# Kernel optimization log

Measured on AMD Instinct MI355X. Metric: run time of the kernel, lower is better.

The kernel has to match this reference:

```python
import jax, jax.numpy as jnp
import numpy as np

N, M, D, DV = 8192, 8192, 128, 128
N_MASK = 1_000_000


def setup_inputs() -> dict:
    key = jax.random.key(0)
    kq, kk, kv, kr, kc = jax.random.split(key, 5)
    query = jax.random.normal(kq, (N, D), dtype=jnp.float32)
    k = jax.random.normal(kk, (M, D), dtype=jnp.float32)
    value = jax.random.normal(kv, (M, DV), dtype=jnp.float32)
    mask_rows = jax.random.randint(kr, (N_MASK,), 0, N, dtype=jnp.int64 if jax.config.jax_enable_x64 else jnp.int32)
    mask_cols = jax.random.randint(kc, (N_MASK,), 0, M, dtype=jnp.int64 if jax.config.jax_enable_x64 else jnp.int32)
    return {"query": query, "key": k, "value": value,
            "mask_rows": mask_rows, "mask_cols": mask_cols}


def reference(query, key, value, mask_rows, mask_cols):
    d = query.shape[1]
    # [N, M] score matrix: q @ k^T / sqrt(d)
    scores = (query @ key.T) / jnp.sqrt(jnp.asarray(d, dtype=query.dtype))
    # scatter -inf at masked coordinates (torch: scaled[mask[0], mask[1]] = -inf)
    scores = scores.at[mask_rows, mask_cols].set(-jnp.inf)
    attn = jax.nn.softmax(scores, axis=1)
    return attn @ value
```

## Files before the change

kernel.cpp:

```cpp
#include <hip/hip_runtime.h>
#include <stdint.h>

#define NQ 8192
#define NM 8192
#define DD 128
#define DVD 128
#define BK 64
#define NKB64 (NM / BK)
#define BQ 128
#define NQB (NQ / BQ)
#define NSPLIT 12

typedef float f32x4 __attribute__((ext_vector_type(4)));
typedef short s16x8 __attribute__((ext_vector_type(8)));
typedef __fp16 fp16x2 __attribute__((ext_vector_type(2)));
union FragU { uint32_t u[4]; s16x8 v; };
union H2U { fp16x2 h; uint32_t u; };

__device__ __forceinline__ uint32_t bf16rne(float x) {
  uint32_t u = __float_as_uint(x);
  return (u + 0x7FFFu + ((u >> 16) & 1u)) >> 16;
}
__device__ __forceinline__ uint32_t pk2(float a, float b) {
  return __builtin_amdgcn_perm(__float_as_uint(b) + 0x8000u,
                               __float_as_uint(a) + 0x8000u, 0x07060302u);
}

__device__ __forceinline__ void glds16(const void* g, void* l) {
  __builtin_amdgcn_global_load_lds((const __attribute__((address_space(1))) uint32_t*)g,
                                   (__attribute__((address_space(3))) uint32_t*)l, 16, 0, 0);
}

#define SZ_MASK ((size_t)(NM / 64) * NQ * 8)
#define OFF_K   (SZ_MASK)
#define SZ_KB   ((size_t)NM * DD * 2)
#define OFF_V   (OFF_K + SZ_KB)
#define OFF_OP  (OFF_V + SZ_KB)
#define SZ_OPH  ((size_t)NQ * DVD * 2)
#define OFF_L   (OFF_OP + (size_t)NSPLIT * SZ_OPH)

__global__ __launch_bounds__(256) void conv_scatter_kernel(
    const float* __restrict__ K, const float* __restrict__ V,
    uint8_t* __restrict__ Kswz, uint8_t* __restrict__ Vtswz,
    const int* __restrict__ mr, const int* __restrict__ mc, int nmask,
    unsigned int* __restrict__ maskT) {
  __shared__ float Vf[64][132];
  int b = blockIdx.x;
  int tid = threadIdx.x;
  if (b < 512) {
    int t = b * 256 + tid;
    int key = t >> 4, c = t & 15;
    const float* s = K + (size_t)key * DD + 8 * c;
    float4 a = *(const float4*)s, bb = *(const float4*)(s + 4);
    uint4 d;
    d.x = bf16rne(a.x) | (bf16rne(a.y) << 16);
    d.y = bf16rne(a.z) | (bf16rne(a.w) << 16);
    d.z = bf16rne(bb.x) | (bf16rne(bb.y) << 16);
    d.w = bf16rne(bb.z) | (bf16rne(bb.w) << 16);
    size_t off = (size_t)(key >> 6) * 16384 + (size_t)(key & 63) * 256 +
                 (size_t)((c ^ (key & 15)) << 4);
    *(uint4*)(Kswz + off) = d;
  } else if (b < 640) {
    int kb = b - 512;
#pragma unroll
    for (int i = 0; i < 8; ++i) {
      int idx = tid + 256 * i;
      int key = idx >> 5, c4 = idx & 31;
      float4 f = *(const float4*)(V + ((size_t)kb * 64 + key) * DVD + 4 * c4);
      *(float4*)&Vf[key][4 * c4] = f;
    }
    __syncthreads();
#pragma unroll
    for (int j = 0; j < 4; ++j) {
      int s = tid + 256 * j;
      int dv = s >> 3, c = s & 7;
      uint4 d;
      uint32_t* dw = (uint32_t*)&d;
#pragma unroll
      for (int w = 0; w < 4; ++w) {
        int k0 = 8 * c + 2 * w;
        dw[w] = bf16rne(Vf[k0][dv]) | (bf16rne(Vf[k0 + 1][dv]) << 16);
      }
      size_t off = (size_t)kb * 16384 + (size_t)dv * 128 + (size_t)((c ^ (dv & 7)) << 4);
      *(uint4*)(Vtswz + off) = d;
    }
  } else {
    size_t i = (size_t)(b - 640) * 256 + tid;
    if (i < (size_t)nmask) {
      int r = mr[i], c = mc[i];
      size_t w = ((size_t)(c >> 6) * NQ + r) * 2 + ((c >> 5) & 1);
      atomicOr(&maskT[w], 1u << (c & 31));
    }
  }
}

__global__ __launch_bounds__(256, 3) void attn_kernel(
    const float* __restrict__ Q, const uint8_t* __restrict__ Kswz,
    const uint8_t* __restrict__ Vtswz, const unsigned int* __restrict__ maskT,
    __fp16* __restrict__ Opart, float* __restrict__ lsum) {
  const int bid = blockIdx.x;
  const int span = bid % NSPLIT;
  const int qblk = bid / NSPLIT;
  const int niter = (span < 8) ? 11 : 10;
  const int kb0 = (span < 8) ? span * 11 : 88 + (span - 8) * 10;

  const int tid = threadIdx.x;
  const int wid = tid >> 6, lane = tid & 63;
  const int g = lane >> 4, qi = lane & 15;
  const int qw = qblk * BQ + wid * 32;

  __shared__ uint8_t Klds[16384];
  __shared__ uint8_t Vlds[16384];
  __shared__ uint32_t Psc[4][16][32];

  const float SC = 0.08838834764831845f * 1.4426950408889634f;

  s16x8 qfrag[2][4];
#pragma unroll
  for (int qt = 0; qt < 2; ++qt)
#pragma unroll
    for (int ks = 0; ks < 4; ++ks) {
      const float* qs = Q + (size_t)(qw + 16 * qt + qi) * DD + 32 * ks + 8 * g;
      float4 a = *(const float4*)qs, b = *(const float4*)(qs + 4);
      FragU fu;
      fu.u[0] = bf16rne(a.x * SC) | (bf16rne(a.y * SC) << 16);
      fu.u[1] = bf16rne(a.z * SC) | (bf16rne(a.w * SC) << 16);
      fu.u[2] = bf16rne(b.x * SC) | (bf16rne(b.y * SC) << 16);
      fu.u[3] = bf16rne(b.z * SC) | (bf16rne(b.w * SC) << 16);
      qfrag[qt][ks] = fu.v;
    }

  f32x4 accO[8][2];
#pragma unroll
  for (int dt = 0; dt < 8; ++dt)
#pragma unroll
    for (int qt = 0; qt < 2; ++qt) accO[dt][qt] = (f32x4)0.f;
  f32x4 accL[2] = {(f32x4)0.f, (f32x4)0.f};
  const f32x4 z4 = (f32x4)0.f;

  FragU onesu;
  onesu.u[0] = onesu.u[1] = onesu.u[2] = onesu.u[3] = 0x3F803F80u;
  const s16x8 onesfrag = onesu.v;

  const s16x8* Kv = (const s16x8*)Klds;
  const s16x8* Vv = (const s16x8*)Vlds;
  const s16x8* kp[4];
#pragma unroll
  for (int ks = 0; ks < 4; ++ks) kp[ks] = Kv + qi * 16 + ((g + 4 * ks) ^ qi);
  const s16x8* vp[2];
#pragma unroll
  for (int kh = 0; kh < 2; ++kh) vp[kh] = Vv + qi * 8 + ((4 * kh + g) ^ (qi & 7));
  uint32_t* pw = &Psc[wid][qi][0];
  uint32_t* wr[4];
#pragma unroll
  for (int kt = 0; kt < 4; ++kt) wr[kt] = &pw[2 * ((4 * kt + g) ^ qi)];
  const uint32_t* rd[4];
#pragma unroll
  for (int kh = 0; kh < 2; ++kh)
#pragma unroll
    for (int hb = 0; hb < 2; ++hb) rd[2 * kh + hb] = &pw[2 * ((8 * kh + 2 * g + hb) ^ qi)];

  const uint8_t* ktp = Kswz + (size_t)kb0 * 16384 + (size_t)tid * 16;
  const uint8_t* vtp = Vtswz + (size_t)kb0 * 16384 + (size_t)tid * 16;
  uint8_t* kld = Klds + wid * 1024;
  uint8_t* vld = Vlds + wid * 1024;
  const uint2* mp0 = (const uint2*)maskT + (size_t)kb0 * NQ + qw + qi;
  const uint2* mp1 = mp0 + 16;

  for (int it = 0; it < niter; ++it) {
    __syncthreads();
#pragma unroll
    for (int s = 0; s < 4; ++s) {
      glds16(ktp + s * 4096, kld + s * 4096);
      glds16(vtp + s * 4096, vld + s * 4096);
    }
    uint2 wm0 = *mp0, wm1 = *mp1;
    ktp += 16384; vtp += 16384; mp0 += NQ; mp1 += NQ;
    __syncthreads();

    f32x4 sf[2][4];
#pragma unroll
    for (int kt = 0; kt < 4; ++kt) {
      {
        s16x8 kf = kp[0][kt * 256];
        sf[0][kt] = __builtin_amdgcn_mfma_f32_16x16x32_bf16(kf, qfrag[0][0], z4, 0, 0, 0);
        sf[1][kt] = __builtin_amdgcn_mfma_f32_16x16x32_bf16(kf, qfrag[1][0], z4, 0, 0, 0);
      }
#pragma unroll
      for (int ks = 1; ks < 4; ++ks) {
        s16x8 kf = kp[ks][kt * 256];
        sf[0][kt] = __builtin_amdgcn_mfma_f32_16x16x32_bf16(kf, qfrag[0][ks], sf[0][kt], 0, 0, 0);
        sf[1][kt] = __builtin_amdgcn_mfma_f32_16x16x32_bf16(kf, qfrag[1][ks], sf[1][kt], 0, 0, 0);
      }
    }

    if (__ballot((wm0.x | wm0.y | wm1.x | wm1.y) != 0)) {
#pragma unroll
      for (int qt = 0; qt < 2; ++qt) {
        uint2 wm = qt ? wm1 : wm0;
#pragma unroll
        for (int kt = 0; kt < 4; ++kt)
#pragma unroll
          for (int r = 0; r < 4; ++r) {
            int kl = 16 * kt + 4 * g + r;
            unsigned int w = (kl & 32) ? wm.y : wm.x;
            if ((w >> (kl & 31)) & 1u) sf[qt][kt][r] = -3.0e38f;
          }
      }
    }

    s16x8 pfrag[2][2];
#pragma unroll
    for (int qt = 0; qt < 2; ++qt) {
#pragma unroll
      for (int kt = 0; kt < 4; ++kt) {
        float p0 = __builtin_amdgcn_exp2f(sf[qt][kt][0]);
        float p1 = __builtin_amdgcn_exp2f(sf[qt][kt][1]);
        float p2 = __builtin_amdgcn_exp2f(sf[qt][kt][2]);
        float p3 = __builtin_amdgcn_exp2f(sf[qt][kt][3]);
        uint2 pk;
        pk.x = pk2(p0, p1);
        pk.y = pk2(p2, p3);
        *(uint2*)wr[kt] = pk;
      }
      FragU pf0, pf1;
      uint2 a0 = *(const uint2*)rd[0];
      uint2 b0 = *(const uint2*)rd[1];
      uint2 a1 = *(const uint2*)rd[2];
      uint2 b1 = *(const uint2*)rd[3];
      pf0.u[0] = a0.x; pf0.u[1] = a0.y; pf0.u[2] = b0.x; pf0.u[3] = b0.y;
      pf1.u[0] = a1.x; pf1.u[1] = a1.y; pf1.u[2] = b1.x; pf1.u[3] = b1.y;
      pfrag[qt][0] = pf0.v;
      pfrag[qt][1] = pf1.v;
    }

#pragma unroll
    for (int kh = 0; kh < 2; ++kh) {
      accL[0] = __builtin_amdgcn_mfma_f32_16x16x32_bf16(onesfrag, pfrag[0][kh], accL[0], 0, 0, 0);
      accL[1] = __builtin_amdgcn_mfma_f32_16x16x32_bf16(onesfrag, pfrag[1][kh], accL[1], 0, 0, 0);
    }

#pragma unroll
    for (int dt = 0; dt < 8; ++dt) {
#pragma unroll
      for (int kh = 0; kh < 2; ++kh) {
        s16x8 vf = vp[kh][dt * 128];
        accO[dt][0] = __builtin_amdgcn_mfma_f32_16x16x32_bf16(vf, pfrag[0][kh], accO[dt][0], 0, 0, 0);
        accO[dt][1] = __builtin_amdgcn_mfma_f32_16x16x32_bf16(vf, pfrag[1][kh], accO[dt][1], 0, 0, 0);
      }
    }
  }

#pragma unroll
  for (int qt = 0; qt < 2; ++qt) {
    int q = qw + 16 * qt + qi;
#pragma unroll
    for (int dt = 0; dt < 8; ++dt) {
      H2U h0, h1;
      h0.h = __builtin_amdgcn_cvt_pkrtz(accO[dt][qt][0], accO[dt][qt][1]);
      h1.h = __builtin_amdgcn_cvt_pkrtz(accO[dt][qt][2], accO[dt][qt][3]);
      uint2 st = {h0.u, h1.u};
      *(uint2*)(Opart + ((size_t)span * NQ + q) * DVD + 16 * dt + 4 * g) = st;
    }
    if (g == 0) lsum[(size_t)span * NQ + q] = accL[qt][0];
  }
}

__global__ __launch_bounds__(256) void merge_kernel(const __fp16* __restrict__ Opart,
                                                    const float* __restrict__ lsum,
                                                    float* __restrict__ out) {
  int idx = blockIdx.x * 256 + threadIdx.x;
  int row = idx >> 5, c4 = idx & 31;
  float den = 0.f;
  f32x4 o = (f32x4)0.f;
#pragma unroll
  for (int p = 0; p < NSPLIT; ++p) {
    den += lsum[(size_t)p * NQ + row];
    uint2 h = *(const uint2*)(Opart + ((size_t)p * NQ + row) * DVD + 4 * c4);
    H2U a, b;
    a.u = h.x; b.u = h.y;
    o[0] += (float)a.h[0]; o[1] += (float)a.h[1];
    o[2] += (float)b.h[0]; o[3] += (float)b.h[1];
  }
  o *= (1.f / den);
  ((f32x4*)out)[idx] = o;
}

extern "C" void kernel_launch(void* const* d_in, const int* in_sizes, int n_in,
                              void* d_out, int out_size, void* d_ws, size_t ws_size,
                              hipStream_t stream) {
  const float* Q = (const float*)d_in[0];
  const float* K = (const float*)d_in[1];
  const float* V = (const float*)d_in[2];
  const int* mr = (const int*)d_in[3];
  const int* mc = (const int*)d_in[4];
  const int nmask = in_sizes[3];

  uint8_t* ws = (uint8_t*)d_ws;
  unsigned int* maskT = (unsigned int*)ws;
  uint8_t* Kswz = ws + OFF_K;
  uint8_t* Vtswz = ws + OFF_V;
  __fp16* Opart = (__fp16*)(ws + OFF_OP);
  float* lsum = (float*)(ws + OFF_L);

  hipMemsetAsync(maskT, 0, SZ_MASK, stream);
  conv_scatter_kernel<<<640 + (nmask + 255) / 256, 256, 0, stream>>>(
      K, V, Kswz, Vtswz, mr, mc, nmask, maskT);
  attn_kernel<<<NQB * NSPLIT, 256, 0, stream>>>(Q, Kswz, Vtswz, maskT, Opart, lsum);
  merge_kernel<<<NQ * DVD / 4 / 256, 256, 0, stream>>>(Opart, lsum, (float*)d_out);
}
```

Measured before the change: 170.2 us.

## Fuse memset, conversion, scatter, attention and merge into one cooperative kernel

Replaces the memset plus three kernel launches with a single cooperative persistent kernel. It uses grid-wide syncs between the phases: mask zeroing with K/V conversion, mask scatter, split attention, and merge. The aim is to remove launch gaps and per-kernel tail drain. The grid is sized from a runtime occupancy query, so the split count is 12 or 8, and the old multi-kernel path remains as a fallback. In exchange, every grid barrier makes all blocks wait on the slowest one. The occupancy query also runs on the host each call, and the merge loop now takes a runtime split count instead of a compile-time one.

```diff
diff --git a/kernel.cpp b/kernel.cpp
--- a/kernel.cpp
+++ b/kernel.cpp
@@ -1,15 +1,15 @@
 #include <hip/hip_runtime.h>
+#include <hip/hip_cooperative_groups.h>
 #include <stdint.h>
+
+namespace cg = cooperative_groups;
 
 #define NQ 8192
 #define NM 8192
 #define DD 128
 #define DVD 128
-#define BK 64
-#define NKB64 (NM / BK)
-#define BQ 128
-#define NQB (NQ / BQ)
-#define NSPLIT 12
+#define NQB 64
+#define NSPLX 12
 
 typedef float f32x4 __attribute__((ext_vector_type(4)));
 typedef short s16x8 __attribute__((ext_vector_type(8)));
@@ -25,7 +25,6 @@
   return __builtin_amdgcn_perm(__float_as_uint(b) + 0x8000u,
                                __float_as_uint(a) + 0x8000u, 0x07060302u);
 }
-
 __device__ __forceinline__ void glds16(const void* g, void* l) {
   __builtin_amdgcn_global_load_lds((const __attribute__((address_space(1))) uint32_t*)g,
                                    (__attribute__((address_space(3))) uint32_t*)l, 16, 0, 0);
@@ -37,18 +36,183 @@
 #define OFF_V   (OFF_K + SZ_KB)
 #define OFF_OP  (OFF_V + SZ_KB)
 #define SZ_OPH  ((size_t)NQ * DVD * 2)
-#define OFF_L   (OFF_OP + (size_t)NSPLIT * SZ_OPH)
-
-__global__ __launch_bounds__(256) void conv_scatter_kernel(
-    const float* __restrict__ K, const float* __restrict__ V,
-    uint8_t* __restrict__ Kswz, uint8_t* __restrict__ Vtswz,
-    const int* __restrict__ mr, const int* __restrict__ mc, int nmask,
-    unsigned int* __restrict__ maskT) {
-  __shared__ float Vf[64][132];
-  int b = blockIdx.x;
-  int tid = threadIdx.x;
-  if (b < 512) {
-    int t = b * 256 + tid;
+#define OFF_L   (OFF_OP + (size_t)NSPLX * SZ_OPH)
+
+struct AttnPtrs {
+  const float* Q;
+  const uint8_t* Kswz;
+  const uint8_t* Vtswz;
+  const unsigned int* maskT;
+  __fp16* Opart;
+  float* lsum;
+};
+
+__device__ __forceinline__ void attn_body(const AttnPtrs& P, uint8_t* smem,
+                                          int tid, int qblk, int span, int kb0,
+                                          int niter) {
+  const int wid = tid >> 6, lane = tid & 63;
+  const int g = lane >> 4, qi = lane & 15;
+  const int qw = qblk * 128 + wid * 32;
+
+  const float SC = 0.08838834764831845f * 1.4426950408889634f;
+
+  s16x8 qfrag[2][4];
+#pragma unroll
+  for (int qt = 0; qt < 2; ++qt)
+#pragma unroll
+    for (int ks = 0; ks < 4; ++ks) {
+      const float* qs = P.Q + (size_t)(qw + 16 * qt + qi) * DD + 32 * ks + 8 * g;
+      float4 a = *(const float4*)qs, b = *(const float4*)(qs + 4);
+      FragU fu;
+      fu.u[0] = bf16rne(a.x * SC) | (bf16rne(a.y * SC) << 16);
+      fu.u[1] = bf16rne(a.z * SC) | (bf16rne(a.w * SC) << 16);
+      fu.u[2] = bf16rne(b.x * SC) | (bf16rne(b.y * SC) << 16);
+      fu.u[3] = bf16rne(b.z * SC) | (bf16rne(b.w * SC) << 16);
+      qfrag[qt][ks] = fu.v;
+    }
+
+  f32x4 accO[8][2];
+#pragma unroll
+  for (int dt = 0; dt < 8; ++dt)
+#pragma unroll
+    for (int qt = 0; qt < 2; ++qt) accO[dt][qt] = (f32x4)0.f;
+  f32x4 accL[2] = {(f32x4)0.f, (f32x4)0.f};
+  const f32x4 z4 = (f32x4)0.f;
+
+  FragU onesu;
+  onesu.u[0] = onesu.u[1] = onesu.u[2] = onesu.u[3] = 0x3F803F80u;
+  const s16x8 onesfrag = onesu.v;
+
+  const s16x8* Kv = (const s16x8*)smem;
+  const s16x8* Vv = (const s16x8*)(smem + 16384);
+  const s16x8* kp[4];
+#pragma unroll
+  for (int ks = 0; ks < 4; ++ks) kp[ks] = Kv + qi * 16 + ((g + 4 * ks) ^ qi);
+  const s16x8* vp[2];
+#pragma unroll
+  for (int kh = 0; kh < 2; ++kh) vp[kh] = Vv + qi * 8 + ((4 * kh + g) ^ (qi & 7));
+  uint32_t* pw = (uint32_t*)(smem + 32768) + (wid * 16 + qi) * 32;
+  uint32_t* wr[4];
+#pragma unroll
+  for (int kt = 0; kt < 4; ++kt) wr[kt] = &pw[2 * ((4 * kt + g) ^ qi)];
+  const uint32_t* rd[4];
+#pragma unroll
+  for (int kh = 0; kh < 2; ++kh)
+#pragma unroll
+    for (int hb = 0; hb < 2; ++hb) rd[2 * kh + hb] = &pw[2 * ((8 * kh + 2 * g + hb) ^ qi)];
+
+  const uint8_t* ktp = P.Kswz + (size_t)kb0 * 16384 + (size_t)tid * 16;
+  const uint8_t* vtp = P.Vtswz + (size_t)kb0 * 16384 + (size_t)tid * 16;
+  uint8_t* kld = smem + wid * 1024;
+  uint8_t* vld = smem + 16384 + wid * 1024;
+  const uint2* mp0 = (const uint2*)P.maskT + (size_t)kb0 * NQ + qw + qi;
+  const uint2* mp1 = mp0 + 16;
+
+  for (int it = 0; it < niter; ++it) {
+    __syncthreads();
+#pragma unroll
+    for (int s = 0; s < 4; ++s) {
+      glds16(ktp + s * 4096, kld + s * 4096);
+      glds16(vtp + s * 4096, vld + s * 4096);
+    }
+    uint2 wm0 = *mp0, wm1 = *mp1;
+    ktp += 16384; vtp += 16384; mp0 += NQ; mp1 += NQ;
+    __syncthreads();
+
+    f32x4 sf[2][4];
+#pragma unroll
+    for (int kt = 0; kt < 4; ++kt) {
+      {
+        s16x8 kf = kp[0][kt * 256];
+        sf[0][kt] = __builtin_amdgcn_mfma_f32_16x16x32_bf16(kf, qfrag[0][0], z4, 0, 0, 0);
+        sf[1][kt] = __builtin_amdgcn_mfma_f32_16x16x32_bf16(kf, qfrag[1][0], z4, 0, 0, 0);
+      }
+#pragma unroll
+      for (int ks = 1; ks < 4; ++ks) {
+        s16x8 kf = kp[ks][kt * 256];
+        sf[0][kt] = __builtin_amdgcn_mfma_f32_16x16x32_bf16(kf, qfrag[0][ks], sf[0][kt], 0, 0, 0);
+        sf[1][kt] = __builtin_amdgcn_mfma_f32_16x16x32_bf16(kf, qfrag[1][ks], sf[1][kt], 0, 0, 0);
+      }
+    }
+
+    if (__ballot((wm0.x | wm0.y | wm1.x | wm1.y) != 0)) {
+#pragma unroll
+      for (int qt = 0; qt < 2; ++qt) {
+        uint2 wm = qt ? wm1 : wm0;
+#pragma unroll
+        for (int kt = 0; kt < 4; ++kt)
+#pragma unroll
+          for (int r = 0; r < 4; ++r) {
+            int kl = 16 * kt + 4 * g + r;
+            unsigned int w = (kl & 32) ? wm.y : wm.x;
+            if ((w >> (kl & 31)) & 1u) sf[qt][kt][r] = -3.0e38f;
+          }
+      }
+    }
+
+    s16x8 pfrag[2][2];
+#pragma unroll
+    for (int qt = 0; qt < 2; ++qt) {
+#pragma unroll
+      for (int kt = 0; kt < 4; ++kt) {
+        float p0 = __builtin_amdgcn_exp2f(sf[qt][kt][0]);
+        float p1 = __builtin_amdgcn_exp2f(sf[qt][kt][1]);
+        float p2 = __builtin_amdgcn_exp2f(sf[qt][kt][2]);
+        float p3 = __builtin_amdgcn_exp2f(sf[qt][kt][3]);
+        uint2 pk;
+        pk.x = pk2(p0, p1);
+        pk.y = pk2(p2, p3);
+        *(uint2*)wr[kt] = pk;
+      }
+      FragU pf0, pf1;
+      uint2 a0 = *(const uint2*)rd[0];
+      uint2 b0 = *(const uint2*)rd[1];
+      uint2 a1 = *(const uint2*)rd[2];
+      uint2 b1 = *(const uint2*)rd[3];
+      pf0.u[0] = a0.x; pf0.u[1] = a0.y; pf0.u[2] = b0.x; pf0.u[3] = b0.y;
+      pf1.u[0] = a1.x; pf1.u[1] = a1.y; pf1.u[2] = b1.x; pf1.u[3] = b1.y;
+      pfrag[qt][0] = pf0.v;
+      pfrag[qt][1] = pf1.v;
+    }
+
+#pragma unroll
+    for (int kh = 0; kh < 2; ++kh) {
+      accL[0] = __builtin_amdgcn_mfma_f32_16x16x32_bf16(onesfrag, pfrag[0][kh], accL[0], 0, 0, 0);
+      accL[1] = __builtin_amdgcn_mfma_f32_16x16x32_bf16(onesfrag, pfrag[1][kh], accL[1], 0, 0, 0);
+    }
+
+#pragma unroll
+    for (int dt = 0; dt < 8; ++dt) {
+#pragma unroll
+      for (int kh = 0; kh < 2; ++kh) {
+        s16x8 vf = vp[kh][dt * 128];
+        accO[dt][0] = __builtin_amdgcn_mfma_f32_16x16x32_bf16(vf, pfrag[0][kh], accO[dt][0], 0, 0, 0);
+        accO[dt][1] = __builtin_amdgcn_mfma_f32_16x16x32_bf16(vf, pfrag[1][kh], accO[dt][1], 0, 0, 0);
+      }
+    }
+  }
+
+#pragma unroll
+  for (int qt = 0; qt < 2; ++qt) {
+    int q = qw + 16 * qt + qi;
+#pragma unroll
+    for (int dt = 0; dt < 8; ++dt) {
+      H2U h0, h1;
+      h0.h = __builtin_amdgcn_cvt_pkrtz(accO[dt][qt][0], accO[dt][qt][1]);
+      h1.h = __builtin_amdgcn_cvt_pkrtz(accO[dt][qt][2], accO[dt][qt][3]);
+      uint2 st = {h0.u, h1.u};
+      *(uint2*)(P.Opart + ((size_t)span * NQ + q) * DVD + 16 * dt + 4 * g) = st;
+    }
+    if (g == 0) P.lsum[(size_t)span * NQ + q] = accL[qt][0];
+  }
+}
+
+__device__ __forceinline__ void conv_vblock(int vb, int tid, const float* K,
+                                            const float* V, uint8_t* Kswz,
+                                            uint8_t* Vtswz, unsigned int* maskT,
+                                            uint8_t* smem) {
+  if (vb < 512) {
+    int t = vb * 256 + tid;
     int key = t >> 4, c = t & 15;
     const float* s = K + (size_t)key * DD + 8 * c;
     float4 a = *(const float4*)s, bb = *(const float4*)(s + 4);
@@ -60,8 +224,9 @@
     size_t off = (size_t)(key >> 6) * 16384 + (size_t)(key & 63) * 256 +
                  (size_t)((c ^ (key & 15)) << 4);
     *(uint4*)(Kswz + off) = d;
-  } else if (b < 640) {
-    int kb = b - 512;
+  } else if (vb < 640) {
+    float(*Vf)[132] = (float(*)[132])smem;
+    int kb = vb - 512;
 #pragma unroll
     for (int i = 0; i < 8; ++i) {
       int idx = tid + 256 * i;
@@ -84,6 +249,82 @@
       size_t off = (size_t)kb * 16384 + (size_t)dv * 128 + (size_t)((c ^ (dv & 7)) << 4);
       *(uint4*)(Vtswz + off) = d;
     }
+    __syncthreads();
+  } else {
+    uint4* m4 = (uint4*)maskT;
+    int i0 = (vb - 640) * 256 + tid;
+    uint4 z = {0, 0, 0, 0};
+#pragma unroll
+    for (int j = 0; j < 16; ++j) m4[i0 + j * 32768] = z;
+  }
+}
+
+__global__ __launch_bounds__(256, 3) void fused_kernel(
+    const float* __restrict__ Q, const float* __restrict__ K,
+    const float* __restrict__ V, const int* __restrict__ mr,
+    const int* __restrict__ mc, int nmask, uint8_t* __restrict__ Kswz,
+    uint8_t* __restrict__ Vtswz, unsigned int* __restrict__ maskT,
+    __fp16* __restrict__ Opart, float* __restrict__ lsum,
+    float* __restrict__ out, int nsplit) {
+  cg::grid_group grid = cg::this_grid();
+  const int bid = blockIdx.x;
+  const int tid = threadIdx.x;
+  const int nthr = gridDim.x * 256;
+  __shared__ uint8_t smem[40960];
+
+  for (int vb = bid; vb < 768; vb += gridDim.x)
+    conv_vblock(vb, tid, K, V, Kswz, Vtswz, maskT, smem);
+  __threadfence();
+  grid.sync();
+
+  for (int i = bid * 256 + tid; i < nmask; i += nthr) {
+    int r = mr[i], c = mc[i];
+    size_t w = ((size_t)(c >> 6) * NQ + r) * 2 + ((c >> 5) & 1);
+    atomicOr(&maskT[w], 1u << (c & 31));
+  }
+  __threadfence();
+  grid.sync();
+
+  {
+    const int span = bid % nsplit;
+    const int qblk = bid / nsplit;
+    const int base = 128 / nsplit;
+    const int rem = 128 - base * nsplit;
+    const int niter = base + (span < rem ? 1 : 0);
+    const int kb0 = span * base + (span < rem ? span : rem);
+    AttnPtrs P = {Q, Kswz, Vtswz, maskT, Opart, lsum};
+    attn_body(P, smem, tid, qblk, span, kb0, niter);
+  }
+  __threadfence();
+  grid.sync();
+
+  for (int idx = bid * 256 + tid; idx < NQ * DVD / 4; idx += nthr) {
+    int row = idx >> 5, c4 = idx & 31;
+    float den = 0.f;
+    f32x4 o = (f32x4)0.f;
+    for (int p = 0; p < nsplit; ++p) {
+      den += lsum[(size_t)p * NQ + row];
+      uint2 h = *(const uint2*)(Opart + ((size_t)p * NQ + row) * DVD + 4 * c4);
+      H2U a, b;
+      a.u = h.x; b.u = h.y;
+      o[0] += (float)a.h[0]; o[1] += (float)a.h[1];
+      o[2] += (float)b.h[0]; o[3] += (float)b.h[1];
+    }
+    o *= (1.f / den);
+    ((f32x4*)out)[idx] = o;
+  }
+}
+
+__global__ __launch_bounds__(256) void conv_scatter_kernel(
+    const float* __restrict__ K, const float* __restrict__ V,
+    uint8_t* __restrict__ Kswz, uint8_t* __restrict__ Vtswz,
+    const int* __restrict__ mr, const int* __restrict__ mc, int nmask,
+    unsigned int* __restrict__ maskT) {
+  __shared__ uint8_t smem[40960];
+  int b = blockIdx.x;
+  int tid = threadIdx.x;
+  if (b < 640) {
+    conv_vblock(b, tid, K, V, Kswz, Vtswz, maskT, smem);
   } else {
     size_t i = (size_t)(b - 640) * 256 + tid;
     if (i < (size_t)nmask) {
@@ -98,172 +339,14 @@
     const float* __restrict__ Q, const uint8_t* __restrict__ Kswz,
     const uint8_t* __restrict__ Vtswz, const unsigned int* __restrict__ maskT,
     __fp16* __restrict__ Opart, float* __restrict__ lsum) {
+  __shared__ uint8_t smem[40960];
   const int bid = blockIdx.x;
-  const int span = bid % NSPLIT;
-  const int qblk = bid / NSPLIT;
+  const int span = bid % 12;
+  const int qblk = bid / 12;
   const int niter = (span < 8) ? 11 : 10;
   const int kb0 = (span < 8) ? span * 11 : 88 + (span - 8) * 10;
-
-  const int tid = threadIdx.x;
-  const int wid = tid >> 6, lane = tid & 63;
-  const int g = lane >> 4, qi = lane & 15;
-  const int qw = qblk * BQ + wid * 32;
-
-  __shared__ uint8_t Klds[16384];
-  __shared__ uint8_t Vlds[16384];
-  __shared__ uint32_t Psc[4][16][32];
-
-  const float SC = 0.08838834764831845f * 1.4426950408889634f;
-
-  s16x8 qfrag[2][4];
-#pragma unroll
-  for (int qt = 0; qt < 2; ++qt)
-#pragma unroll
-    for (int ks = 0; ks < 4; ++ks) {
-      const float* qs = Q + (size_t)(qw + 16 * qt + qi) * DD + 32 * ks + 8 * g;
-      float4 a = *(const float4*)qs, b = *(const float4*)(qs + 4);
-      FragU fu;
-      fu.u[0] = bf16rne(a.x * SC) | (bf16rne(a.y * SC) << 16);
-      fu.u[1] = bf16rne(a.z * SC) | (bf16rne(a.w * SC) << 16);
-      fu.u[2] = bf16rne(b.x * SC) | (bf16rne(b.y * SC) << 16);
-      fu.u[3] = bf16rne(b.z * SC) | (bf16rne(b.w * SC) << 16);
-      qfrag[qt][ks] = fu.v;
-    }
-
-  f32x4 accO[8][2];
-#pragma unroll
-  for (int dt = 0; dt < 8; ++dt)
-#pragma unroll
-    for (int qt = 0; qt < 2; ++qt) accO[dt][qt] = (f32x4)0.f;
-  f32x4 accL[2] = {(f32x4)0.f, (f32x4)0.f};
-  const f32x4 z4 = (f32x4)0.f;
-
-  FragU onesu;
-  onesu.u[0] = onesu.u[1] = onesu.u[2] = onesu.u[3] = 0x3F803F80u;
-  const s16x8 onesfrag = onesu.v;
-
-  const s16x8* Kv = (const s16x8*)Klds;
-  const s16x8* Vv = (const s16x8*)Vlds;
-  const s16x8* kp[4];
-#pragma unroll
-  for (int ks = 0; ks < 4; ++ks) kp[ks] = Kv + qi * 16 + ((g + 4 * ks) ^ qi);
-  const s16x8* vp[2];
-#pragma unroll
-  for (int kh = 0; kh < 2; ++kh) vp[kh] = Vv + qi * 8 + ((4 * kh + g) ^ (qi & 7));
-  uint32_t* pw = &Psc[wid][qi][0];
-  uint32_t* wr[4];
-#pragma unroll
-  for (int kt = 0; kt < 4; ++kt) wr[kt] = &pw[2 * ((4 * kt + g) ^ qi)];
-  const uint32_t* rd[4];
-#pragma unroll
-  for (int kh = 0; kh < 2; ++kh)
-#pragma unroll
-    for (int hb = 0; hb < 2; ++hb) rd[2 * kh + hb] = &pw[2 * ((8 * kh + 2 * g + hb) ^ qi)];
-
-  const uint8_t* ktp = Kswz + (size_t)kb0 * 16384 + (size_t)tid * 16;
-  const uint8_t* vtp = Vtswz + (size_t)kb0 * 16384 + (size_t)tid * 16;
-  uint8_t* kld = Klds + wid * 1024;
-  uint8_t* vld = Vlds + wid * 1024;
-  const uint2* mp0 = (const uint2*)maskT + (size_t)kb0 * NQ + qw + qi;
-  const uint2* mp1 = mp0 + 16;
-
-  for (int it = 0; it < niter; ++it) {
-    __syncthreads();
-#pragma unroll
-    for (int s = 0; s < 4; ++s) {
-      glds16(ktp + s * 4096, kld + s * 4096);
-      glds16(vtp + s * 4096, vld + s * 4096);
-    }
-    uint2 wm0 = *mp0, wm1 = *mp1;
-    ktp += 16384; vtp += 16384; mp0 += NQ; mp1 += NQ;
-    __syncthreads();
-
-    f32x4 sf[2][4];
-#pragma unroll
-    for (int kt = 0; kt < 4; ++kt) {
-      {
-        s16x8 kf = kp[0][kt * 256];
-        sf[0][kt] = __builtin_amdgcn_mfma_f32_16x16x32_bf16(kf, qfrag[0][0], z4, 0, 0, 0);
-        sf[1][kt] = __builtin_amdgcn_mfma_f32_16x16x32_bf16(kf, qfrag[1][0], z4, 0, 0, 0);
-      }
-#pragma unroll
-      for (int ks = 1; ks < 4; ++ks) {
-        s16x8 kf = kp[ks][kt * 256];
-        sf[0][kt] = __builtin_amdgcn_mfma_f32_16x16x32_bf16(kf, qfrag[0][ks], sf[0][kt], 0, 0, 0);
-        sf[1][kt] = __builtin_amdgcn_mfma_f32_16x16x32_bf16(kf, qfrag[1][ks], sf[1][kt], 0, 0, 0);
-      }
-    }
-
-    if (__ballot((wm0.x | wm0.y | wm1.x | wm1.y) != 0)) {
-#pragma unroll
-      for (int qt = 0; qt < 2; ++qt) {
-        uint2 wm = qt ? wm1 : wm0;
-#pragma unroll
-        for (int kt = 0; kt < 4; ++kt)
-#pragma unroll
-          for (int r = 0; r < 4; ++r) {
-            int kl = 16 * kt + 4 * g + r;
-            unsigned int w = (kl & 32) ? wm.y : wm.x;
-            if ((w >> (kl & 31)) & 1u) sf[qt][kt][r] = -3.0e38f;
-          }
-      }
-    }
-
-    s16x8 pfrag[2][2];
-#pragma unroll
-    for (int qt = 0; qt < 2; ++qt) {
-#pragma unroll
-      for (int kt = 0; kt < 4; ++kt) {
-        float p0 = __builtin_amdgcn_exp2f(sf[qt][kt][0]);
-        float p1 = __builtin_amdgcn_exp2f(sf[qt][kt][1]);
-        float p2 = __builtin_amdgcn_exp2f(sf[qt][kt][2]);
-        float p3 = __builtin_amdgcn_exp2f(sf[qt][kt][3]);
-        uint2 pk;
-        pk.x = pk2(p0, p1);
-        pk.y = pk2(p2, p3);
-        *(uint2*)wr[kt] = pk;
-      }
-      FragU pf0, pf1;
-      uint2 a0 = *(const uint2*)rd[0];
-      uint2 b0 = *(const uint2*)rd[1];
-      uint2 a1 = *(const uint2*)rd[2];
-      uint2 b1 = *(const uint2*)rd[3];
-      pf0.u[0] = a0.x; pf0.u[1] = a0.y; pf0.u[2] = b0.x; pf0.u[3] = b0.y;
-      pf1.u[0] = a1.x; pf1.u[1] = a1.y; pf1.u[2] = b1.x; pf1.u[3] = b1.y;
-      pfrag[qt][0] = pf0.v;
-      pfrag[qt][1] = pf1.v;
-    }
-
-#pragma unroll
-    for (int kh = 0; kh < 2; ++kh) {
-      accL[0] = __builtin_amdgcn_mfma_f32_16x16x32_bf16(onesfrag, pfrag[0][kh], accL[0], 0, 0, 0);
-      accL[1] = __builtin_amdgcn_mfma_f32_16x16x32_bf16(onesfrag, pfrag[1][kh], accL[1], 0, 0, 0);
-    }
-
-#pragma unroll
-    for (int dt = 0; dt < 8; ++dt) {
-#pragma unroll
-      for (int kh = 0; kh < 2; ++kh) {
-        s16x8 vf = vp[kh][dt * 128];
-        accO[dt][0] = __builtin_amdgcn_mfma_f32_16x16x32_bf16(vf, pfrag[0][kh], accO[dt][0], 0, 0, 0);
-        accO[dt][1] = __builtin_amdgcn_mfma_f32_16x16x32_bf16(vf, pfrag[1][kh], accO[dt][1], 0, 0, 0);
-      }
-    }
-  }
-
-#pragma unroll
-  for (int qt = 0; qt < 2; ++qt) {
-    int q = qw + 16 * qt + qi;
-#pragma unroll
-    for (int dt = 0; dt < 8; ++dt) {
-      H2U h0, h1;
-      h0.h = __builtin_amdgcn_cvt_pkrtz(accO[dt][qt][0], accO[dt][qt][1]);
-      h1.h = __builtin_amdgcn_cvt_pkrtz(accO[dt][qt][2], accO[dt][qt][3]);
-      uint2 st = {h0.u, h1.u};
-      *(uint2*)(Opart + ((size_t)span * NQ + q) * DVD + 16 * dt + 4 * g) = st;
-    }
-    if (g == 0) lsum[(size_t)span * NQ + q] = accL[qt][0];
-  }
+  AttnPtrs P = {Q, Kswz, Vtswz, maskT, Opart, lsum};
+  attn_body(P, smem, threadIdx.x, qblk, span, kb0, niter);
 }
 
 __global__ __launch_bounds__(256) void merge_kernel(const __fp16* __restrict__ Opart,
@@ -274,7 +357,7 @@
   float den = 0.f;
   f32x4 o = (f32x4)0.f;
 #pragma unroll
-  for (int p = 0; p < NSPLIT; ++p) {
+  for (int p = 0; p < 12; ++p) {
     den += lsum[(size_t)p * NQ + row];
     uint2 h = *(const uint2*)(Opart + ((size_t)p * NQ + row) * DVD + 4 * c4);
     H2U a, b;
@@ -294,7 +377,7 @@
   const float* V = (const float*)d_in[2];
   const int* mr = (const int*)d_in[3];
   const int* mc = (const int*)d_in[4];
-  const int nmask = in_sizes[3];
+  int nmask = in_sizes[3];
 
   uint8_t* ws = (uint8_t*)d_ws;
   unsigned int* maskT = (unsigned int*)ws;
@@ -302,10 +385,31 @@
   uint8_t* Vtswz = ws + OFF_V;
   __fp16* Opart = (__fp16*)(ws + OFF_OP);
   float* lsum = (float*)(ws + OFF_L);
+  float* outp = (float*)d_out;
+
+  int occ = 0;
+  hipError_t qe = hipOccupancyMaxActiveBlocksPerMultiprocessor(&occ, fused_kernel, 256, 0);
+  int nsplit = 0;
+  if (qe == hipSuccess) {
+    if (occ >= 3) nsplit = 12;
+    else if (occ == 2) nsplit = 8;
+  }
+  if (nsplit) {
+    int grid = NQB * nsplit;
+    void* args[] = {(void*)&Q,     (void*)&K,     (void*)&V,    (void*)&mr,
+                    (void*)&mc,    (void*)&nmask, (void*)&Kswz, (void*)&Vtswz,
+                    (void*)&maskT, (void*)&Opart, (void*)&lsum, (void*)&outp,
+                    (void*)&nsplit};
+    hipError_t le = hipLaunchCooperativeKernel((const void*)fused_kernel, dim3(grid),
+                                               dim3(256), args, 0, stream);
+    if (le == hipSuccess) {
+      return;
+    }
+  }
 
   hipMemsetAsync(maskT, 0, SZ_MASK, stream);
   conv_scatter_kernel<<<640 + (nmask + 255) / 256, 256, 0, stream>>>(
       K, V, Kswz, Vtswz, mr, mc, nmask, maskT);
-  attn_kernel<<<NQB * NSPLIT, 256, 0, stream>>>(Q, Kswz, Vtswz, maskT, Opart, lsum);
+  attn_kernel<<<NQB * 12, 256, 0, stream>>>(Q, Kswz, Vtswz, maskT, Opart, lsum);
   merge_kernel<<<NQ * DVD / 4 / 256, 256, 0, stream>>>(Opart, lsum, (float*)d_out);
 }
```

Measured after the change: 170.3 us. No clear change (+0.0%).

## Halve key tile to 32 and double-buffer K/V LDS loads

Applied to the files above, without the earlier changes.

Shrinks the key block from 64 to 32 keys and changes the K/V swizzled layouts, the mask bitmap (one word per 32 keys) and the split schedule to match. Uses the freed LDS for a two-stage ping-pong buffer, so the next tile's global-to-LDS loads and mask words are issued before computing on the current tile. This removes one barrier per iteration and hides load latency. The cost is twice as many iterations, with more loop overhead and fewer MFMAs per barrier.

```diff
diff --git a/kernel.cpp b/kernel.cpp
--- a/kernel.cpp
+++ b/kernel.cpp
@@ -5,10 +5,7 @@
 #define NM 8192
 #define DD 128
 #define DVD 128
-#define BK 64
-#define NKB64 (NM / BK)
-#define BQ 128
-#define NQB (NQ / BQ)
+#define NQB 64
 #define NSPLIT 12
 
 typedef float f32x4 __attribute__((ext_vector_type(4)));
@@ -25,13 +22,12 @@
   return __builtin_amdgcn_perm(__float_as_uint(b) + 0x8000u,
                                __float_as_uint(a) + 0x8000u, 0x07060302u);
 }
-
 __device__ __forceinline__ void glds16(const void* g, void* l) {
   __builtin_amdgcn_global_load_lds((const __attribute__((address_space(1))) uint32_t*)g,
                                    (__attribute__((address_space(3))) uint32_t*)l, 16, 0, 0);
 }
 
-#define SZ_MASK ((size_t)(NM / 64) * NQ * 8)
+#define SZ_MASK ((size_t)(NM / 32) * NQ * 4)
 #define OFF_K   (SZ_MASK)
 #define SZ_KB   ((size_t)NM * DD * 2)
 #define OFF_V   (OFF_K + SZ_KB)
@@ -44,7 +40,7 @@
     uint8_t* __restrict__ Kswz, uint8_t* __restrict__ Vtswz,
     const int* __restrict__ mr, const int* __restrict__ mc, int nmask,
     unsigned int* __restrict__ maskT) {
-  __shared__ float Vf[64][132];
+  __shared__ float Vf[32][132];
   int b = blockIdx.x;
   int tid = threadIdx.x;
   if (b < 512) {
@@ -57,23 +53,23 @@
     d.y = bf16rne(a.z) | (bf16rne(a.w) << 16);
     d.z = bf16rne(bb.x) | (bf16rne(bb.y) << 16);
     d.w = bf16rne(bb.z) | (bf16rne(bb.w) << 16);
-    size_t off = (size_t)(key >> 6) * 16384 + (size_t)(key & 63) * 256 +
+    size_t off = (size_t)(key >> 5) * 8192 + (size_t)(key & 31) * 256 +
                  (size_t)((c ^ (key & 15)) << 4);
     *(uint4*)(Kswz + off) = d;
-  } else if (b < 640) {
+  } else if (b < 768) {
     int kb = b - 512;
 #pragma unroll
-    for (int i = 0; i < 8; ++i) {
+    for (int i = 0; i < 4; ++i) {
       int idx = tid + 256 * i;
       int key = idx >> 5, c4 = idx & 31;
-      float4 f = *(const float4*)(V + ((size_t)kb * 64 + key) * DVD + 4 * c4);
+      float4 f = *(const float4*)(V + ((size_t)kb * 32 + key) * DVD + 4 * c4);
       *(float4*)&Vf[key][4 * c4] = f;
     }
     __syncthreads();
 #pragma unroll
-    for (int j = 0; j < 4; ++j) {
+    for (int j = 0; j < 2; ++j) {
       int s = tid + 256 * j;
-      int dv = s >> 3, c = s & 7;
+      int dv = s >> 2, c = s & 3;
       uint4 d;
       uint32_t* dw = (uint32_t*)&d;
 #pragma unroll
@@ -81,15 +77,14 @@
         int k0 = 8 * c + 2 * w;
         dw[w] = bf16rne(Vf[k0][dv]) | (bf16rne(Vf[k0 + 1][dv]) << 16);
       }
-      size_t off = (size_t)kb * 16384 + (size_t)dv * 128 + (size_t)((c ^ (dv & 7)) << 4);
+      size_t off = (size_t)kb * 8192 + (size_t)dv * 64 + (size_t)((c ^ (dv & 3)) << 4);
       *(uint4*)(Vtswz + off) = d;
     }
   } else {
-    size_t i = (size_t)(b - 640) * 256 + tid;
+    size_t i = (size_t)(b - 768) * 256 + tid;
     if (i < (size_t)nmask) {
       int r = mr[i], c = mc[i];
-      size_t w = ((size_t)(c >> 6) * NQ + r) * 2 + ((c >> 5) & 1);
-      atomicOr(&maskT[w], 1u << (c & 31));
+      atomicOr(&maskT[(size_t)(c >> 5) * NQ + r], 1u << (c & 31));
     }
   }
 }
@@ -101,17 +96,18 @@
   const int bid = blockIdx.x;
   const int span = bid % NSPLIT;
   const int qblk = bid / NSPLIT;
-  const int niter = (span < 8) ? 11 : 10;
-  const int kb0 = (span < 8) ? span * 11 : 88 + (span - 8) * 10;
+  const int niter = (span < 4) ? 22 : 21;
+  const int kb0 = (span < 4) ? span * 22 : 88 + (span - 4) * 21;
 
   const int tid = threadIdx.x;
   const int wid = tid >> 6, lane = tid & 63;
   const int g = lane >> 4, qi = lane & 15;
-  const int qw = qblk * BQ + wid * 32;
-
-  __shared__ uint8_t Klds[16384];
-  __shared__ uint8_t Vlds[16384];
-  __shared__ uint32_t Psc[4][16][32];
+  const int qw = qblk * 128 + wid * 32;
+
+  __shared__ uint8_t smem[36864];
+  uint8_t* Klds = smem;
+  uint8_t* Vlds = smem + 16384;
+  uint32_t* Psc = (uint32_t*)(smem + 32768);
 
   const float SC = 0.08838834764831845f * 1.4426950408889634f;
 
@@ -142,78 +138,88 @@
   onesu.u[0] = onesu.u[1] = onesu.u[2] = onesu.u[3] = 0x3F803F80u;
   const s16x8 onesfrag = onesu.v;
 
-  const s16x8* Kv = (const s16x8*)Klds;
-  const s16x8* Vv = (const s16x8*)Vlds;
-  const s16x8* kp[4];
-#pragma unroll
-  for (int ks = 0; ks < 4; ++ks) kp[ks] = Kv + qi * 16 + ((g + 4 * ks) ^ qi);
-  const s16x8* vp[2];
-#pragma unroll
-  for (int kh = 0; kh < 2; ++kh) vp[kh] = Vv + qi * 8 + ((4 * kh + g) ^ (qi & 7));
-  uint32_t* pw = &Psc[wid][qi][0];
-  uint32_t* wr[4];
-#pragma unroll
-  for (int kt = 0; kt < 4; ++kt) wr[kt] = &pw[2 * ((4 * kt + g) ^ qi)];
-  const uint32_t* rd[4];
-#pragma unroll
-  for (int kh = 0; kh < 2; ++kh)
-#pragma unroll
-    for (int hb = 0; hb < 2; ++hb) rd[2 * kh + hb] = &pw[2 * ((8 * kh + 2 * g + hb) ^ qi)];
-
-  const uint8_t* ktp = Kswz + (size_t)kb0 * 16384 + (size_t)tid * 16;
-  const uint8_t* vtp = Vtswz + (size_t)kb0 * 16384 + (size_t)tid * 16;
+  const s16x8* kp0[4];
+#pragma unroll
+  for (int ks = 0; ks < 4; ++ks)
+    kp0[ks] = (const s16x8*)Klds + qi * 16 + ((g + 4 * ks) ^ qi);
+  const s16x8* vp0 = (const s16x8*)Vlds + qi * 4 + (g ^ (qi & 3));
+  uint32_t* pw = Psc + (wid * 16 + qi) * 16;
+  uint32_t* wr[2];
+#pragma unroll
+  for (int kt = 0; kt < 2; ++kt) wr[kt] = &pw[2 * ((4 * kt + g) ^ (qi & 7))];
+  const uint32_t* rd[2];
+#pragma unroll
+  for (int hb = 0; hb < 2; ++hb) rd[hb] = &pw[2 * ((2 * g + hb) ^ (qi & 7))];
+
+  const uint8_t* ktp = Kswz + (size_t)kb0 * 8192 + (size_t)tid * 16;
+  const uint8_t* vtp = Vtswz + (size_t)kb0 * 8192 + (size_t)tid * 16;
   uint8_t* kld = Klds + wid * 1024;
   uint8_t* vld = Vlds + wid * 1024;
-  const uint2* mp0 = (const uint2*)maskT + (size_t)kb0 * NQ + qw + qi;
-  const uint2* mp1 = mp0 + 16;
+  const uint32_t* mq = maskT + (size_t)kb0 * NQ + qw + qi;
+
+  {
+    glds16(ktp, kld);
+    glds16(ktp + 4096, kld + 4096);
+    glds16(vtp, vld);
+    glds16(vtp + 4096, vld + 4096);
+    ktp += 8192; vtp += 8192;
+  }
+  uint32_t wmc0 = mq[0], wmc1 = mq[16];
+  const uint32_t* mqn = mq + NQ;
 
   for (int it = 0; it < niter; ++it) {
     __syncthreads();
-#pragma unroll
-    for (int s = 0; s < 4; ++s) {
-      glds16(ktp + s * 4096, kld + s * 4096);
-      glds16(vtp + s * 4096, vld + s * 4096);
-    }
-    uint2 wm0 = *mp0, wm1 = *mp1;
-    ktp += 16384; vtp += 16384; mp0 += NQ; mp1 += NQ;
-    __syncthreads();
-
-    f32x4 sf[2][4];
-#pragma unroll
-    for (int kt = 0; kt < 4; ++kt) {
+    const int par = it & 1;
+    const int nxt = it + 1 < niter;
+    if (nxt) {
+      uint8_t* kldn = kld + (par ? 0 : 8192);
+      uint8_t* vldn = vld + (par ? 0 : 8192);
+      glds16(ktp, kldn);
+      glds16(ktp + 4096, kldn + 4096);
+      glds16(vtp, vldn);
+      glds16(vtp + 4096, vldn + 4096);
+      ktp += 8192; vtp += 8192;
+    }
+    uint32_t wmn0 = mqn[0], wmn1 = mqn[16];
+    if (nxt) mqn += NQ;
+
+    const int kofs = par * 512;
+    f32x4 sf[2][2];
+#pragma unroll
+    for (int kt = 0; kt < 2; ++kt) {
       {
-        s16x8 kf = kp[0][kt * 256];
+        s16x8 kf = kp0[0][kofs + kt * 256];
         sf[0][kt] = __builtin_amdgcn_mfma_f32_16x16x32_bf16(kf, qfrag[0][0], z4, 0, 0, 0);
         sf[1][kt] = __builtin_amdgcn_mfma_f32_16x16x32_bf16(kf, qfrag[1][0], z4, 0, 0, 0);
       }
 #pragma unroll
       for (int ks = 1; ks < 4; ++ks) {
-        s16x8 kf = kp[ks][kt * 256];
+        s16x8 kf = kp0[ks][kofs + kt * 256];
         sf[0][kt] = __builtin_amdgcn_mfma_f32_16x16x32_bf16(kf, qfrag[0][ks], sf[0][kt], 0, 0, 0);
         sf[1][kt] = __builtin_amdgcn_mfma_f32_16x16x32_bf16(kf, qfrag[1][ks], sf[1][kt], 0, 0, 0);
       }
     }
 
-    if (__ballot((wm0.x | wm0.y | wm1.x | wm1.y) != 0)) {
+    if (__ballot((wmc0 | wmc1) != 0)) {
 #pragma unroll
       for (int qt = 0; qt < 2; ++qt) {
-        uint2 wm = qt ? wm1 : wm0;
-#pragma unroll
-        for (int kt = 0; kt < 4; ++kt)
+        uint32_t wm = qt ? wmc1 : wmc0;
+#pragma unroll
+        for (int kt = 0; kt < 2; ++kt)
 #pragma unroll
           for (int r = 0; r < 4; ++r) {
             int kl = 16 * kt + 4 * g + r;
-            unsigned int w = (kl & 32) ? wm.y : wm.x;
-            if ((w >> (kl & 31)) & 1u) sf[qt][kt][r] = -3.0e38f;
+            if ((wm >> kl) & 1u) sf[qt][kt][r] = -3.0e38f;
           }
       }
     }
-
-    s16x8 pfrag[2][2];
+    wmc0 = wmn0; wmc1 = wmn1;
+
+    s16x8 pfrag[2];
 #pragma unroll
     for (int qt = 0; qt < 2; ++qt) {
 #pragma unroll
-      for (int kt = 0; kt < 4; ++kt) {
+      for (int kt = 0; kt < 2; ++kt) {
         float p0 = __builtin_amdgcn_exp2f(sf[qt][kt][0]);
         float p1 = __builtin_amdgcn_exp2f(sf[qt][kt][1]);
         float p2 = __builtin_amdgcn_exp2f(sf[qt][kt][2]);
@@ -223,31 +229,21 @@
         pk.y = pk2(p2, p3);
         *(uint2*)wr[kt] = pk;
       }
-      FragU pf0, pf1;
       uint2 a0 = *(const uint2*)rd[0];
       uint2 b0 = *(const uint2*)rd[1];
-      uint2 a1 = *(const uint2*)rd[2];
-      uint2 b1 = *(const uint2*)rd[3];
-      pf0.u[0] = a0.x; pf0.u[1] = a0.y; pf0.u[2] = b0.x; pf0.u[3] = b0.y;
-      pf1.u[0] = a1.x; pf1.u[1] = a1.y; pf1.u[2] = b1.x; pf1.u[3] = b1.y;
-      pfrag[qt][0] = pf0.v;
-      pfrag[qt][1] = pf1.v;
-    }
-
-#pragma unroll
-    for (int kh = 0; kh < 2; ++kh) {
-      accL[0] = __builtin_amdgcn_mfma_f32_16x16x32_bf16(onesfrag, pfrag[0][kh], accL[0], 0, 0, 0);
-      accL[1] = __builtin_amdgcn_mfma_f32_16x16x32_bf16(onesfrag, pfrag[1][kh], accL[1], 0, 0, 0);
-    }
+      FragU pf;
+      pf.u[0] = a0.x; pf.u[1] = a0.y; pf.u[2] = b0.x; pf.u[3] = b0.y;
+      pfrag[qt] = pf.v;
+    }
+
+    accL[0] = __builtin_amdgcn_mfma_f32_16x16x32_bf16(onesfrag, pfrag[0], accL[0], 0, 0, 0);
+    accL[1] = __builtin_amdgcn_mfma_f32_16x16x32_bf16(onesfrag, pfrag[1], accL[1], 0, 0, 0);
 
 #pragma unroll
     for (int dt = 0; dt < 8; ++dt) {
-#pragma unroll
-      for (int kh = 0; kh < 2; ++kh) {
-        s16x8 vf = vp[kh][dt * 128];
-        accO[dt][0] = __builtin_amdgcn_mfma_f32_16x16x32_bf16(vf, pfrag[0][kh], accO[dt][0], 0, 0, 0);
-        accO[dt][1] = __builtin_amdgcn_mfma_f32_16x16x32_bf16(vf, pfrag[1][kh], accO[dt][1], 0, 0, 0);
-      }
+      s16x8 vf = vp0[kofs + dt * 64];
+      accO[dt][0] = __builtin_amdgcn_mfma_f32_16x16x32_bf16(vf, pfrag[0], accO[dt][0], 0, 0, 0);
+      accO[dt][1] = __builtin_amdgcn_mfma_f32_16x16x32_bf16(vf, pfrag[1], accO[dt][1], 0, 0, 0);
     }
   }
 
@@ -294,7 +290,7 @@
   const float* V = (const float*)d_in[2];
   const int* mr = (const int*)d_in[3];
   const int* mc = (const int*)d_in[4];
-  const int nmask = in_sizes[3];
+  int nmask = in_sizes[3];
 
   uint8_t* ws = (uint8_t*)d_ws;
   unsigned int* maskT = (unsigned int*)ws;
@@ -304,7 +300,7 @@
   float* lsum = (float*)(ws + OFF_L);
 
   hipMemsetAsync(maskT, 0, SZ_MASK, stream);
-  conv_scatter_kernel<<<640 + (nmask + 255) / 256, 256, 0, stream>>>(
+  conv_scatter_kernel<<<768 + (nmask + 255) / 256, 256, 0, stream>>>(
       K, V, Kswz, Vtswz, mr, mc, nmask, maskT);
   attn_kernel<<<NQB * NSPLIT, 256, 0, stream>>>(Q, Kswz, Vtswz, maskT, Opart, lsum);
   merge_kernel<<<NQ * DVD / 4 / 256, 256, 0, stream>>>(Opart, lsum, (float*)d_out);
```

After: 166.7 us. 1.02x faster.
